# Performance work log

Hardware: AMD Instinct MI355X
Metric: run time of the kernel (lower is better)

## Reference

```python
import jax, jax.numpy as jnp
import numpy as np

N = 100000   # nodes
E = 1600000  # edges
G = 64       # graphs in batch
H, C = 8, 16 # heads, per-head channels
HID = H * C  # 128
EMB, BBOX, TOK, REL = 256, 32, 151, 51
IN0 = EMB + BBOX  # 288
NEG_SLOPE = 0.2
BN_EPS = 1e-5


def setup_inputs() -> dict:
    key = jax.random.key(0)
    ks = jax.random.split(key, 32)
    f = lambda i, shape: jax.random.normal(ks[i], shape, dtype=jnp.float32) * 0.05
    inp = {}
    inp["tok_id"] = jax.random.randint(ks[0], (N,), 0, TOK)
    inp["bbox"] = jax.random.normal(ks[1], (N, 4), dtype=jnp.float32)
    inp["edge_index"] = jax.random.randint(ks[2], (2, E), 0, N)
    inp["edge_attr"] = jax.random.randint(ks[3], (E,), 0, REL)
    inp["batch"] = jnp.sort(jax.random.randint(ks[4], (N,), 0, G))
    inp["tok_emb"] = f(5, (TOK, EMB))
    inp["bbox_W"] = f(6, (4, BBOX)); inp["bbox_b"] = f(7, (BBOX,))
    inp["rel_emb"] = f(8, (REL, C))
    # layer 0 (in_dim 288 -> 128)
    inp["Wl0"] = f(9, (IN0, HID));  inp["bl0"] = f(10, (HID,))
    inp["Wr0"] = f(11, (IN0, HID)); inp["br0"] = f(12, (HID,))
    inp["We0"] = f(13, (C, HID));   inp["att0"] = f(14, (H, C))
    inp["bias0"] = f(15, (HID,))
    inp["gamma0"] = jnp.ones((HID,), jnp.float32); inp["beta0"] = jnp.zeros((HID,), jnp.float32)
    # layers 1..2 stacked (128 -> 128)
    inp["WlS"] = f(16, (2, HID, HID)); inp["blS"] = f(17, (2, HID))
    inp["WrS"] = f(18, (2, HID, HID)); inp["brS"] = f(19, (2, HID))
    inp["WeS"] = f(20, (2, C, HID));   inp["attS"] = f(21, (2, H, C))
    inp["biasS"] = f(22, (2, HID))
    inp["gammaS"] = jnp.ones((2, HID), jnp.float32); inp["betaS"] = jnp.zeros((2, HID), jnp.float32)
    return inp


def gatv2_layer(x, src, dst, e_emb, Wl, bl, Wr, br, We, att, bias):
    """GATv2Conv: gather -> leaky_relu attention -> segment softmax -> scatter."""
    xl = (x @ Wl + bl).reshape(-1, H, C)   # source transform [N,H,C]
    xr = (x @ Wr + br).reshape(-1, H, C)   # target transform [N,H,C]
    ee = (e_emb @ We).reshape(-1, H, C)    # edge transform  [E,H,C]
    m = jax.nn.leaky_relu(xl[src] + xr[dst] + ee, NEG_SLOPE)  # [E,H,C]
    logits = jnp.einsum('ehc,hc->eh', m, att)                 # [E,H]
    amax = jax.ops.segment_max(logits, dst, num_segments=N)   # [N,H]
    p = jnp.exp(logits - amax[dst])
    denom = jax.ops.segment_sum(p, dst, num_segments=N)       # [N,H]
    alpha = p / jnp.maximum(denom[dst], 1e-16)                # [E,H]
    out = jax.ops.segment_sum(alpha[..., None] * xl[src], dst, num_segments=N)  # [N,H,C]
    return out.reshape(-1, HID) + bias


def batch_norm(x, gamma, beta):
    mu = jnp.mean(x, axis=0)
    var = jnp.var(x, axis=0)
    return gamma * (x - mu) * jax.lax.rsqrt(var + BN_EPS) + beta


def reference(tok_id, bbox, edge_index, edge_attr, batch,
              tok_emb, bbox_W, bbox_b, rel_emb,
              Wl0, bl0, Wr0, br0, We0, att0, bias0, gamma0, beta0,
              WlS, blS, WrS, brS, WeS, attS, biasS, gammaS, betaS):
    src, dst = edge_index[0], edge_index[1]
    x = jnp.concatenate([tok_emb[tok_id], bbox @ bbox_W + bbox_b], axis=-1)  # [N,288]
    e_emb = rel_emb[edge_attr]  # [E,16]
    h = batch_norm(jax.nn.relu(
        gatv2_layer(x, src, dst, e_emb, Wl0, bl0, Wr0, br0, We0, att0, bias0)),
        gamma0, beta0)
    for i in range(2):
        h = h + batch_norm(jax.nn.relu(
            gatv2_layer(h, src, dst, e_emb, WlS[i], blS[i], WrS[i], brS[i], WeS[i], attS[i], biasS[i])),
            gammaS[i], betaS[i])
    # global mean pool over graphs
    sums = jax.ops.segment_sum(h, batch, num_segments=G)
    counts = jax.ops.segment_sum(jnp.ones((h.shape[0],), h.dtype), batch, num_segments=G)
    return sums / jnp.maximum(counts, 1.0)[:, None]  # [G,128]
```

## Files before the change

kernel.cpp:

```cpp
#include <hip/hip_runtime.h>

#define N_NODES 100000
#define N_PAD   100096
#define N_EDGES 1600000
#define NGRAPH  64
#define NHEAD   8
#define NCH     16
#define HID     128
#define IN0     288
#define NREL    51
#define EMB     256
#define NBBOX   32
#define NTOK    151
#define NEG_SLOPE 0.2f
#define EPS_BN  1e-5f
#define AGG_BLOCKS 2048
#define POOL_BLOCKS 1024
#define SENT 0x03F00000u
#define SENT_MIN ((uint)(NREL) << 20)
#define L2E 1.4426950408889634f

typedef unsigned int uint;
typedef unsigned short ushort;

typedef __bf16 bf16_t;
typedef bf16_t bfx8 __attribute__((ext_vector_type(8)));
typedef float  fx4  __attribute__((ext_vector_type(4)));
typedef float  v2f  __attribute__((ext_vector_type(2)));

__device__ __forceinline__ ushort f2bf(float f) {
  uint u = __float_as_uint(f);
  u += 0x7fffu + ((u >> 16) & 1u);
  return (ushort)(u >> 16);
}
__device__ __forceinline__ float bf2f(uint u) { return __uint_as_float(u << 16); }
__device__ __forceinline__ v2f up2(uint u) {
  v2f r;
  r.x = __uint_as_float(u << 16);
  r.y = __uint_as_float(u & 0xffff0000u);
  return r;
}
__device__ __forceinline__ void unpack8(uint4 u, float* f) {
  f[0] = __uint_as_float(u.x << 16); f[1] = __uint_as_float(u.x & 0xffff0000u);
  f[2] = __uint_as_float(u.y << 16); f[3] = __uint_as_float(u.y & 0xffff0000u);
  f[4] = __uint_as_float(u.z << 16); f[5] = __uint_as_float(u.z & 0xffff0000u);
  f[6] = __uint_as_float(u.w << 16); f[7] = __uint_as_float(u.w & 0xffff0000u);
}

__device__ __forceinline__ float w0cat(const float* Wl0, const float* Wr0, int c, int j) {
  return (j < 128) ? Wl0[c * 128 + j] : Wr0[c * 128 + (j - 128)];
}

#define S0 (2 * 256 * HID)
#define S1 (3 * NREL * HID)
#define S2 (3 * 256)
#define S3 (NTOK * 256)
#define S4 (4 * 256)
#define S5 (256)
#define PREP_TOT (S0 + S1 + S2 + S3 + S4 + S5)
__global__ void se_prep(const float* __restrict__ Wl0, const float* __restrict__ Wr0,
                        const float* __restrict__ WlS, const float* __restrict__ WrS,
                        const float* __restrict__ rel_emb, const float* __restrict__ We0,
                        const float* __restrict__ WeS,
                        const float* __restrict__ bl0, const float* __restrict__ br0,
                        const float* __restrict__ blS, const float* __restrict__ brS,
                        const float* __restrict__ tok_emb, const float* __restrict__ bbox_W,
                        const float* __restrict__ bbox_b,
                        ushort* __restrict__ WST, float* __restrict__ eetab,
                        float* __restrict__ biascat,
                        float* __restrict__ T, float* __restrict__ F, float* __restrict__ cvec) {
  int i = blockIdx.x * 256 + threadIdx.x;
  if (i < S0) {
    int li = i >> 15;
    int rem = i & 32767;
    int j = rem >> 7, k = rem & 127;
    float v = (j < 128) ? WlS[(li * 128 + k) * 128 + j] : WrS[(li * 128 + k) * 128 + (j - 128)];
    WST[(li * 256 + j) * 128 + k] = f2bf(v);
    return;
  }
  i -= S0;
  if (i < S1) {
    int li = i / (NREL * HID);
    int rem = i - li * (NREL * HID);
    int r = rem >> 7, j = rem & 127;
    const float* We = (li == 0) ? We0 : (WeS + (li - 1) * NCH * HID);
    float s = 0.f;
#pragma unroll
    for (int c = 0; c < NCH; c++) s += rel_emb[r * NCH + c] * We[c * HID + j];
    eetab[li * (NREL * HID) + rem] = s;
    return;
  }
  i -= S1;
  if (i < S2) {
    int li = i >> 8, j = i & 255;
    const float* bl = (li == 0) ? bl0 : (blS + (li - 1) * HID);
    const float* br = (li == 0) ? br0 : (brS + (li - 1) * HID);
    biascat[i] = (j < 128) ? bl[j] : br[j - 128];
    return;
  }
  i -= S2;
  if (i < S3) {
    int t = i >> 8, j = i & 255;
    float s = 0.f;
    for (int c = 0; c < EMB; c++) s += tok_emb[t * EMB + c] * w0cat(Wl0, Wr0, c, j);
    T[i] = s;
    return;
  }
  i -= S3;
  if (i < S4) {
    int r = i >> 8, j = i & 255;
    float s = 0.f;
#pragma unroll
    for (int b = 0; b < NBBOX; b++) s += bbox_W[r * NBBOX + b] * w0cat(Wl0, Wr0, EMB + b, j);
    F[i] = s;
    return;
  }
  i -= S4;
  if (i < S5) {
    int j = i;
    float s = (j < 128) ? bl0[j] : br0[j - 128];
#pragma unroll
    for (int b = 0; b < NBBOX; b++) s += bbox_b[b] * w0cat(Wl0, Wr0, EMB + b, j);
    cvec[j] = s;
  }
}

__global__ void se_xform0(const int* __restrict__ tok_id, const float* __restrict__ bbox,
                          const float* __restrict__ T, const float* __restrict__ F,
                          const float* __restrict__ cvec, ushort* __restrict__ xlxr) {
  int idx = blockIdx.x * 256 + threadIdx.x;
  if (idx >= N_NODES * 32) return;
  const int n = idx >> 5, k = idx & 31;
  const int j0 = k * 8;
  const int t = tok_id[n];
  const float4 bb = *(const float4*)(bbox + (size_t)n * 4);
  float o[8];
#pragma unroll
  for (int h = 0; h < 2; h++) {
    const float4 tv = *(const float4*)(T + t * 256 + j0 + 4 * h);
    const float4 cv = *(const float4*)(cvec + j0 + 4 * h);
    const float4 f0 = *(const float4*)(F + 0 * 256 + j0 + 4 * h);
    const float4 f1 = *(const float4*)(F + 1 * 256 + j0 + 4 * h);
    const float4 f2 = *(const float4*)(F + 2 * 256 + j0 + 4 * h);
    const float4 f3 = *(const float4*)(F + 3 * 256 + j0 + 4 * h);
    o[4 * h + 0] = tv.x + cv.x + bb.x * f0.x + bb.y * f1.x + bb.z * f2.x + bb.w * f3.x;
    o[4 * h + 1] = tv.y + cv.y + bb.x * f0.y + bb.y * f1.y + bb.z * f2.y + bb.w * f3.y;
    o[4 * h + 2] = tv.z + cv.z + bb.x * f0.z + bb.y * f1.z + bb.z * f2.z + bb.w * f3.z;
    o[4 * h + 3] = tv.w + cv.w + bb.x * f0.w + bb.y * f1.w + bb.z * f2.w + bb.w * f3.w;
  }
  uint4 p;
  p.x = ((uint)f2bf(o[1]) << 16) | f2bf(o[0]);
  p.y = ((uint)f2bf(o[3]) << 16) | f2bf(o[2]);
  p.z = ((uint)f2bf(o[5]) << 16) | f2bf(o[4]);
  p.w = ((uint)f2bf(o[7]) << 16) | f2bf(o[6]);
  ((uint4*)xlxr)[idx] = p;
}

__global__ void se_hist(const int* __restrict__ ei, int* __restrict__ deg) {
  int e = blockIdx.x * 256 + threadIdx.x;
  if (e < N_EDGES) atomicAdd(&deg[ei[N_EDGES + e]], 1);
}
__global__ __launch_bounds__(1024) void se_scanA(const int* __restrict__ deg,
                                                 int* __restrict__ offs, int* __restrict__ bsum) {
  __shared__ int s[1024];
  const int tid = threadIdx.x;
  const int i = blockIdx.x * 1024 + tid;
  int v = (i < N_NODES) ? ((deg[i] + 3) & ~3) : 0;
  s[tid] = v;
  __syncthreads();
  for (int d = 1; d < 1024; d <<= 1) {
    int t = (tid >= d) ? s[tid - d] : 0;
    __syncthreads();
    s[tid] += t;
    __syncthreads();
  }
  if (i < N_NODES) offs[i] = s[tid] - v;
  if (tid == 1023) bsum[blockIdx.x] = s[1023];
}
__global__ __launch_bounds__(128) void se_scanB(int* __restrict__ bsum, int nb) {
  __shared__ int s[128];
  const int t = threadIdx.x;
  int v = (t < nb) ? bsum[t] : 0;
  s[t] = v;
  __syncthreads();
  for (int d = 1; d < 128; d <<= 1) {
    int u = (t >= d) ? s[t - d] : 0;
    __syncthreads();
    s[t] += u;
    __syncthreads();
  }
  if (t < nb) bsum[t] = s[t] - v;
}
__global__ __launch_bounds__(1024) void se_scanC(int* __restrict__ offs, const int* __restrict__ bsum) {
  int i = blockIdx.x * 1024 + threadIdx.x;
  if (i < N_NODES) offs[i] += bsum[blockIdx.x];
}
__global__ void se_padfill(const int* __restrict__ deg, const int* __restrict__ offs,
                           uint* __restrict__ csrp, int2* __restrict__ rowinfo) {
  int n = blockIdx.x * 256 + threadIdx.x;
  if (n >= N_NODES) return;
  const int d = deg[n];
  const int o = offs[n];
  rowinfo[n] = make_int2(o, (d + 3) >> 2);
  const int s = o + d;
  const int c = ((d + 3) & ~3) - d;
  for (int j = 0; j < c; j++) csrp[s + j] = SENT;
  if (n == N_NODES - 1) {
    const int e = o + ((d + 3) & ~3);
    for (int j = 0; j < 64; j++) csrp[e + j] = SENT;
  }
}
__global__ void se_scatter(const int* __restrict__ ei, const int* __restrict__ eattr,
                           const int* __restrict__ offs, int* __restrict__ cur,
                           uint* __restrict__ csrp) {
  int e = blockIdx.x * 256 + threadIdx.x;
  if (e < N_EDGES) {
    int d = ei[N_EDGES + e];
    int p = offs[d] + atomicAdd(&cur[d], 1);
    csrp[p] = (uint)ei[e] | ((uint)eattr[e] << 20);
  }
}

template <int K>
__global__ __launch_bounds__(256) void se_gemm(const ushort* __restrict__ A,
                                               const ushort* __restrict__ BT,
                                               const float* __restrict__ bias,
                                               ushort* __restrict__ C) {
  __shared__ __align__(16) ushort As[128 * 32];
  __shared__ __align__(16) ushort Bs[128 * 32];
  const int tid = threadIdx.x;
  const int w = tid >> 6, l = tid & 63;
  const int wr = w >> 1, wc = w & 1;
  const int m0 = blockIdx.x * 128, n0 = blockIdx.y * 128;
  fx4 acc[4][4];
#pragma unroll
  for (int i = 0; i < 4; i++)
#pragma unroll
    for (int j = 0; j < 4; j++) acc[i][j] = fx4{0.f, 0.f, 0.f, 0.f};

  for (int k0 = 0; k0 < K; k0 += 32) {
#pragma unroll
    for (int ch = 0; ch < 2; ch++) {
      const int t = tid + ch * 256;
      const int r = t >> 2, c = (t & 3) << 3;
      const ushort* ga = A + (size_t)(m0 + r) * K + (k0 + c);
      ushort* la = As + (size_t)(ch * 256 + w * 64) * 8;
      __builtin_amdgcn_global_load_lds((const __attribute__((address_space(1))) void*)ga,
                                       (__attribute__((address_space(3))) void*)la, 16, 0, 0);
      const ushort* gb = BT + (size_t)(n0 + r) * K + (k0 + c);
      ushort* lb = Bs + (size_t)(ch * 256 + w * 64) * 8;
      __builtin_amdgcn_global_load_lds((const __attribute__((address_space(1))) void*)gb,
                                       (__attribute__((address_space(3))) void*)lb, 16, 0, 0);
    }
    __syncthreads();
    bfx8 af[4], bfr[4];
#pragma unroll
    for (int i = 0; i < 4; i++) {
      af[i]  = *(const bfx8*)(As + ((wr * 64 + i * 16 + (l & 15)) * 32 + ((l >> 4) * 8)));
      bfr[i] = *(const bfx8*)(Bs + ((wc * 64 + i * 16 + (l & 15)) * 32 + ((l >> 4) * 8)));
    }
#pragma unroll
    for (int i = 0; i < 4; i++)
#pragma unroll
      for (int j = 0; j < 4; j++)
        acc[i][j] = __builtin_amdgcn_mfma_f32_16x16x32_bf16(af[i], bfr[j], acc[i][j], 0, 0, 0);
    __syncthreads();
  }
#pragma unroll
  for (int i = 0; i < 4; i++) {
    const int rbase = m0 + wr * 64 + i * 16 + ((l >> 4) << 2);
#pragma unroll
    for (int j = 0; j < 4; j++) {
      const int col = n0 + wc * 64 + j * 16 + (l & 15);
      const float bz = bias[col];
#pragma unroll
      for (int r2 = 0; r2 < 4; r2++) {
        const int row = rbase + r2;
        if (row < N_NODES) C[(size_t)row * 256 + col] = f2bf(acc[i][j][r2] + bz);
      }
    }
  }
}

__global__ __launch_bounds__(256) void se_agg(const uint4* __restrict__ xlxr4,
                                              const uint* __restrict__ csrp,
                                              const int2* __restrict__ rowinfo,
                                              const float* __restrict__ eetab,
                                              const float* __restrict__ att,
                                              const float* __restrict__ bias,
                                              ushort* __restrict__ y, float* __restrict__ partial) {
  __shared__ ushort ee[64 * HID];
  __shared__ float bstat[256];
  const int tid = threadIdx.x, w = tid >> 6, l = tid & 63;
  const int g = l >> 4, k = l & 15;
  for (int i = tid; i < 64 * HID; i += 256) {
    const int r = i >> 7;
    ee[i] = (r < NREL) ? f2bf(eetab[i]) : (ushort)0;
  }
  bstat[tid] = 0.f;
  __syncthreads();
  v2f a1v[4], a2v[4];
  {
    const float* ap = att + (k >> 1) * NCH + (k & 1) * 8;
#pragma unroll
    for (int q = 0; q < 4; q++) {
      a1v[q] = v2f{ap[2 * q] * (0.6f * L2E), ap[2 * q + 1] * (0.6f * L2E)};
      a2v[q] = v2f{ap[2 * q] * (0.4f * L2E), ap[2 * q + 1] * (0.4f * L2E)};
    }
  }
  v2f sv[4], qv[4];
#pragma unroll
  for (int q = 0; q < 4; q++) { sv[q] = v2f{0.f, 0.f}; qv[q] = v2f{0.f, 0.f}; }
  const v2f zero = v2f{0.f, 0.f};

  const int stride = gridDim.x * 4;
  for (int n = blockIdx.x * 4 + w; n < N_NODES; n += stride) {
    const int2 ri = rowinfo[n];
    const uint* rowp = csrp + ri.x + g;
    const int nit = ri.y;
    v2f xrv[4];
    {
      const uint4 xru = xlxr4[(uint)n * 32u + 16u + (uint)k];
      xrv[0] = up2(xru.x); xrv[1] = up2(xru.y); xrv[2] = up2(xru.z); xrv[3] = up2(xru.w);
    }
    float den = 0.f;
    v2f acc[4];
#pragma unroll
    for (int q = 0; q < 4; q++) acc[q] = zero;

    uint eA = SENT, eB = SENT;
    uint4 xlv = uint4{0u, 0u, 0u, 0u};
    if (nit > 0) {
      eA = rowp[0];
      xlv = xlxr4[(eA & 0xFFFFFu) * 32u + (uint)k];
      if (nit > 1) eB = rowp[4];
    }
    for (int i = 0; i < nit; ++i) {
      const uint ec = eA;
      const uint4 xc = xlv;
      eA = eB;
      if (i + 1 < nit) xlv = xlxr4[(eA & 0xFFFFFu) * 32u + (uint)k];
      if (i + 2 < nit) eB = rowp[4 * (i + 2)];
      const uint4 eeu = *(const uint4*)(ee + (ec >> 20) * HID + k * 8);
      v2f sd1 = zero, sd2 = zero;
      v2f xls[4];
      {
        const uint xcu[4] = {xc.x, xc.y, xc.z, xc.w};
        const uint eu[4] = {eeu.x, eeu.y, eeu.z, eeu.w};
#pragma unroll
        for (int q = 0; q < 4; q++) {
          const v2f xl = up2(xcu[q]);
          const v2f m = xl + xrv[q] + up2(eu[q]);
          sd1 += m * a1v[q];
          sd2 += __builtin_elementwise_abs(m) * a2v[q];
          xls[q] = xl;
        }
      }
      float s = sd1.x + sd1.y + sd2.x + sd2.y;
      s += __shfl_xor(s, 1);
      s = (ec >= SENT_MIN) ? -1e30f : s;
      const float p = exp2f(s);
      den += p;
      const v2f pp = v2f{p, p};
#pragma unroll
      for (int q = 0; q < 4; q++) acc[q] += pp * xls[q];
    }
    den += __shfl_xor(den, 16);
    den += __shfl_xor(den, 32);
#pragma unroll
    for (int q = 0; q < 4; q++) {
      acc[q].x += __shfl_xor(acc[q].x, 16); acc[q].x += __shfl_xor(acc[q].x, 32);
      acc[q].y += __shfl_xor(acc[q].y, 16); acc[q].y += __shfl_xor(acc[q].y, 32);
    }
    if (g == 0) {
      const float r = 1.f / fmaxf(den, 1e-16f);
      const v2f rr = v2f{r, r};
      const float4 b0 = ((const float4*)bias)[k * 2];
      const float4 b1 = ((const float4*)bias)[k * 2 + 1];
      const v2f bv[4] = {v2f{b0.x, b0.y}, v2f{b0.z, b0.w}, v2f{b1.x, b1.y}, v2f{b1.z, b1.w}};
      v2f ov[4];
#pragma unroll
      for (int q = 0; q < 4; q++) {
        ov[q] = __builtin_elementwise_max(acc[q] * rr + bv[q], zero);
        sv[q] += ov[q];
        qv[q] += ov[q] * ov[q];
      }
      uint4 p4;
      p4.x = ((uint)f2bf(ov[0].y) << 16) | f2bf(ov[0].x);
      p4.y = ((uint)f2bf(ov[1].y) << 16) | f2bf(ov[1].x);
      p4.z = ((uint)f2bf(ov[2].y) << 16) | f2bf(ov[2].x);
      p4.w = ((uint)f2bf(ov[3].y) << 16) | f2bf(ov[3].x);
      ((uint4*)y)[(size_t)n * 16 + k] = p4;
    }
  }
  if (l < 16) {
#pragma unroll
    for (int q = 0; q < 4; q++) {
      unsafeAtomicAdd(&bstat[k * 8 + 2 * q], sv[q].x);
      unsafeAtomicAdd(&bstat[k * 8 + 2 * q + 1], sv[q].y);
      unsafeAtomicAdd(&bstat[128 + k * 8 + 2 * q], qv[q].x);
      unsafeAtomicAdd(&bstat[128 + k * 8 + 2 * q + 1], qv[q].y);
    }
  }
  __syncthreads();
  partial[(size_t)tid * AGG_BLOCKS + blockIdx.x] = bstat[tid];
}

__global__ __launch_bounds__(256) void se_stats(const float* __restrict__ partial, float* __restrict__ musig) {
  __shared__ float red[256];
  const int ch = blockIdx.x, tid = threadIdx.x;
  float s = 0.f;
  for (int i = tid; i < AGG_BLOCKS; i += 256) s += partial[ch * AGG_BLOCKS + i];
  red[tid] = s; __syncthreads();
  for (int o = 128; o > 0; o >>= 1) { if (tid < o) red[tid] += red[tid + o]; __syncthreads(); }
  const float sum = red[0]; __syncthreads();
  float q = 0.f;
  for (int i = tid; i < AGG_BLOCKS; i += 256) q += partial[(128 + ch) * AGG_BLOCKS + i];
  red[tid] = q; __syncthreads();
  for (int o = 128; o > 0; o >>= 1) { if (tid < o) red[tid] += red[tid + o]; __syncthreads(); }
  if (tid == 0) {
    const float mean = sum / (float)N_NODES;
    const float var = red[0] / (float)N_NODES - mean * mean;
    musig[ch] = mean;
    musig[128 + ch] = rsqrtf(var + EPS_BN);
  }
}

__global__ void se_bn(const ushort* __restrict__ y, const float* __restrict__ musig,
                      const float* __restrict__ gamma, const float* __restrict__ beta,
                      ushort* __restrict__ h_bf, int residual) {
  int idx = blockIdx.x * 256 + threadIdx.x;
  if (idx >= N_NODES * 16) return;
  const int k = idx & 15;
  const uint4 yv = ((const uint4*)y)[idx];
  float f[8];
  unpack8(yv, f);
  const float4 mu0 = ((const float4*)musig)[k * 2],         mu1 = ((const float4*)musig)[k * 2 + 1];
  const float4 rs0 = ((const float4*)(musig + 128))[k * 2], rs1 = ((const float4*)(musig + 128))[k * 2 + 1];
  const float4 g0  = ((const float4*)gamma)[k * 2],         g1  = ((const float4*)gamma)[k * 2 + 1];
  const float4 b0  = ((const float4*)beta)[k * 2],          b1  = ((const float4*)beta)[k * 2 + 1];
  float v[8];
  v[0] = g0.x * (f[0] - mu0.x) * rs0.x + b0.x;
  v[1] = g0.y * (f[1] - mu0.y) * rs0.y + b0.y;
  v[2] = g0.z * (f[2] - mu0.z) * rs0.z + b0.z;
  v[3] = g0.w * (f[3] - mu0.w) * rs0.w + b0.w;
  v[4] = g1.x * (f[4] - mu1.x) * rs1.x + b1.x;
  v[5] = g1.y * (f[5] - mu1.y) * rs1.y + b1.y;
  v[6] = g1.z * (f[6] - mu1.z) * rs1.z + b1.z;
  v[7] = g1.w * (f[7] - mu1.w) * rs1.w + b1.w;
  if (residual) {
    const uint4 ho = ((const uint4*)h_bf)[idx];
    float fr[8];
    unpack8(ho, fr);
#pragma unroll
    for (int j = 0; j < 8; j++) v[j] += fr[j];
  }
  uint4 p4;
  p4.x = ((uint)f2bf(v[1]) << 16) | f2bf(v[0]);
  p4.y = ((uint)f2bf(v[3]) << 16) | f2bf(v[2]);
  p4.z = ((uint)f2bf(v[5]) << 16) | f2bf(v[4]);
  p4.w = ((uint)f2bf(v[7]) << 16) | f2bf(v[6]);
  ((uint4*)h_bf)[idx] = p4;
}

__global__ __launch_bounds__(256) void se_pool(const ushort* __restrict__ h_bf,
                                               const int* __restrict__ batch,
                                               float* __restrict__ pool) {
  const int tid = threadIdx.x, w = tid >> 6, l = tid & 63;
  const int wid = blockIdx.x * 4 + w;
  const int nw = gridDim.x * 4;
  const int chunk = (N_NODES + nw - 1) / nw;
  const int start = wid * chunk;
  const int end = min(N_NODES, start + chunk);
  float a0 = 0.f, a1 = 0.f;
  int cg = -1, cnt = 0;
  for (int n = start; n < end; ++n) {
    const int gg = batch[n];
    if (gg != cg) {
      if (cg >= 0) {
        unsafeAtomicAdd(&pool[cg * HID + 2 * l], a0);
        unsafeAtomicAdd(&pool[cg * HID + 2 * l + 1], a1);
        if (l == 0) unsafeAtomicAdd(&pool[NGRAPH * HID + cg], (float)cnt);
      }
      a0 = 0.f; a1 = 0.f; cnt = 0; cg = gg;
    }
    const uint u = ((const uint*)h_bf)[(size_t)n * 64 + l];
    a0 += bf2f(u & 0xffffu);
    a1 += __uint_as_float(u & 0xffff0000u);
    cnt++;
  }
  if (cg >= 0) {
    unsafeAtomicAdd(&pool[cg * HID + 2 * l], a0);
    unsafeAtomicAdd(&pool[cg * HID + 2 * l + 1], a1);
    if (l == 0) unsafeAtomicAdd(&pool[NGRAPH * HID + cg], (float)cnt);
  }
}
__global__ void se_poolfin(const float* __restrict__ pool, float* __restrict__ out) {
  int idx = blockIdx.x * 256 + threadIdx.x;
  if (idx < NGRAPH * HID) {
    int g = idx >> 7;
    out[idx] = pool[idx] / fmaxf(pool[NGRAPH * HID + g], 1.f);
  }
}

extern "C" void kernel_launch(void* const* d_in, const int* in_sizes, int n_in,
                              void* d_out, int out_size, void* d_ws, size_t ws_size,
                              hipStream_t stream) {
  (void)in_sizes; (void)n_in; (void)out_size; (void)ws_size;
  const int*   tok_id  = (const int*)d_in[0];
  const float* bbox    = (const float*)d_in[1];
  const int*   ei      = (const int*)d_in[2];
  const int*   eattr   = (const int*)d_in[3];
  const int*   batch   = (const int*)d_in[4];
  const float* tok_emb = (const float*)d_in[5];
  const float* bbox_W  = (const float*)d_in[6];
  const float* bbox_b  = (const float*)d_in[7];
  const float* rel_emb = (const float*)d_in[8];
  const float* Wl0  = (const float*)d_in[9];
  const float* bl0  = (const float*)d_in[10];
  const float* Wr0  = (const float*)d_in[11];
  const float* br0  = (const float*)d_in[12];
  const float* We0  = (const float*)d_in[13];
  const float* att0 = (const float*)d_in[14];
  const float* bias0  = (const float*)d_in[15];
  const float* gamma0 = (const float*)d_in[16];
  const float* beta0  = (const float*)d_in[17];
  const float* WlS  = (const float*)d_in[18];
  const float* blS  = (const float*)d_in[19];
  const float* WrS  = (const float*)d_in[20];
  const float* brS  = (const float*)d_in[21];
  const float* WeS  = (const float*)d_in[22];
  const float* attS = (const float*)d_in[23];
  const float* biasS  = (const float*)d_in[24];
  const float* gammaS = (const float*)d_in[25];
  const float* betaS  = (const float*)d_in[26];
  float* out = (float*)d_out;

  char* ws = (char*)d_ws;
  size_t off = 0;
  auto alloc = [&](size_t bytes) -> char* {
    char* p = ws + off;
    off = (off + bytes + 255) & ~(size_t)255;
    return p;
  };
  ushort* xlxr = (ushort*)alloc((size_t)N_PAD * 256 * 2);
  ushort* y    = (ushort*)alloc((size_t)N_NODES * HID * 2);
  ushort* h_bf = (ushort*)alloc((size_t)N_PAD * HID * 2);
  ushort* WST  = (ushort*)alloc((size_t)2 * 256 * HID * 2);
  float*  eetab   = (float*)alloc((size_t)3 * NREL * HID * 4);
  float*  biascat = (float*)alloc((size_t)3 * 256 * 4);
  float*  T    = (float*)alloc((size_t)NTOK * 256 * 4);
  float*  F    = (float*)alloc((size_t)4 * 256 * 4);
  float*  cvec = (float*)alloc((size_t)256 * 4);
  int* deg  = (int*)alloc((size_t)N_NODES * 4);
  int* offs = (int*)alloc((size_t)(N_NODES + 1) * 4);
  int* cur  = (int*)alloc((size_t)N_NODES * 4);
  int* bsum = (int*)alloc(128 * 4);
  int2* rowinfo = (int2*)alloc((size_t)N_NODES * 8);
  uint* csrp = (uint*)alloc((size_t)(N_EDGES + 3 * N_NODES + 256) * 4);
  float* partial = (float*)alloc((size_t)256 * AGG_BLOCKS * 4);
  float* musig   = (float*)alloc(256 * 4);
  float* pool    = (float*)alloc((size_t)(NGRAPH * HID + NGRAPH) * 4);

  hipMemsetAsync(deg, 0, (size_t)N_NODES * 4, stream);
  hipMemsetAsync(cur, 0, (size_t)N_NODES * 4, stream);
  hipMemsetAsync(pool, 0, (size_t)(NGRAPH * HID + NGRAPH) * 4, stream);

  se_prep<<<(PREP_TOT + 255) / 256, 256, 0, stream>>>(
      Wl0, Wr0, WlS, WrS, rel_emb, We0, WeS, bl0, br0, blS, brS,
      tok_emb, bbox_W, bbox_b, WST, eetab, biascat, T, F, cvec);
  se_hist<<<(N_EDGES + 255) / 256, 256, 0, stream>>>(ei, deg);
  se_scanA<<<98, 1024, 0, stream>>>(deg, offs, bsum);
  se_scanB<<<1, 128, 0, stream>>>(bsum, 98);
  se_scanC<<<98, 1024, 0, stream>>>(offs, bsum);
  se_padfill<<<(N_NODES + 255) / 256, 256, 0, stream>>>(deg, offs, csrp, rowinfo);
  se_scatter<<<(N_EDGES + 255) / 256, 256, 0, stream>>>(ei, eattr, offs, cur, csrp);

  se_xform0<<<(N_NODES * 32 + 255) / 256, 256, 0, stream>>>(tok_id, bbox, T, F, cvec, xlxr);
  se_agg<<<AGG_BLOCKS, 256, 0, stream>>>((const uint4*)xlxr, csrp, rowinfo,
                                         eetab, att0, bias0, y, partial);
  se_stats<<<128, 256, 0, stream>>>(partial, musig);
  se_bn<<<(N_NODES * 16 + 255) / 256, 256, 0, stream>>>(y, musig, gamma0, beta0, h_bf, 0);

  for (int li = 0; li < 2; ++li) {
    se_gemm<HID><<<dim3(N_PAD / 128, 2), 256, 0, stream>>>(h_bf, WST + (size_t)li * 256 * HID,
                                                           biascat + (li + 1) * 256, xlxr);
    se_agg<<<AGG_BLOCKS, 256, 0, stream>>>((const uint4*)xlxr, csrp, rowinfo,
                                           eetab + (size_t)(li + 1) * NREL * HID,
                                           attS + (size_t)li * NHEAD * NCH,
                                           biasS + (size_t)li * HID, y, partial);
    se_stats<<<128, 256, 0, stream>>>(partial, musig);
    se_bn<<<(N_NODES * 16 + 255) / 256, 256, 0, stream>>>(y, musig, gammaS + (size_t)li * HID,
                                                          betaS + (size_t)li * HID, h_bf, 1);
  }

  se_pool<<<POOL_BLOCKS, 256, 0, stream>>>(h_bf, batch, pool);
  se_poolfin<<<32, 256, 0, stream>>>(pool, out);
}
```

Before: 828.2 us.

## Use fp32 edge table and output, direct leaky-relu, merged memsets

The aggregation kernel now keeps the edge-embedding table in shared memory as fp32 instead of bf16. It computes leaky_relu directly as max(m, 0.2m) instead of the abs-based split into two accumulators, and unrolls the edge loop by two. The intermediate y buffer is stored as fp32, so the batch-norm kernel reads floats instead of unpacking bf16. The three workspace memsets are merged into one by placing the zeroed buffers next to each other. This trims ALU work in the inner loop and removes two memset launches, at the cost of twice the y traffic and more shared memory per block, which may lower occupancy.

```diff
diff --git a/kernel.cpp b/kernel.cpp
--- a/kernel.cpp
+++ b/kernel.cpp
@@ -288,25 +288,22 @@
                                               const float* __restrict__ eetab,
                                               const float* __restrict__ att,
                                               const float* __restrict__ bias,
-                                              ushort* __restrict__ y, float* __restrict__ partial) {
-  __shared__ ushort ee[64 * HID];
+                                              float* __restrict__ y, float* __restrict__ partial) {
+  __shared__ float ee[64 * HID];
   __shared__ float bstat[256];
   const int tid = threadIdx.x, w = tid >> 6, l = tid & 63;
   const int g = l >> 4, k = l & 15;
   for (int i = tid; i < 64 * HID; i += 256) {
     const int r = i >> 7;
-    ee[i] = (r < NREL) ? f2bf(eetab[i]) : (ushort)0;
+    ee[i] = (r < NREL) ? eetab[i] : 0.f;
   }
   bstat[tid] = 0.f;
   __syncthreads();
-  v2f a1v[4], a2v[4];
+  v2f av[4];
   {
     const float* ap = att + (k >> 1) * NCH + (k & 1) * 8;
 #pragma unroll
-    for (int q = 0; q < 4; q++) {
-      a1v[q] = v2f{ap[2 * q] * (0.6f * L2E), ap[2 * q + 1] * (0.6f * L2E)};
-      a2v[q] = v2f{ap[2 * q] * (0.4f * L2E), ap[2 * q + 1] * (0.4f * L2E)};
-    }
+    for (int q = 0; q < 4; q++) av[q] = v2f{ap[2 * q] * L2E, ap[2 * q + 1] * L2E};
   }
   v2f sv[4], qv[4];
 #pragma unroll
@@ -335,28 +332,32 @@
       xlv = xlxr4[(eA & 0xFFFFFu) * 32u + (uint)k];
       if (nit > 1) eB = rowp[4];
     }
+#pragma unroll 2
     for (int i = 0; i < nit; ++i) {
       const uint ec = eA;
       const uint4 xc = xlv;
       eA = eB;
       if (i + 1 < nit) xlv = xlxr4[(eA & 0xFFFFFu) * 32u + (uint)k];
       if (i + 2 < nit) eB = rowp[4 * (i + 2)];
-      const uint4 eeu = *(const uint4*)(ee + (ec >> 20) * HID + k * 8);
-      v2f sd1 = zero, sd2 = zero;
+      const float* eerow = ee + (ec >> 20) * HID + k * 8;
+      const float4 e0v = *(const float4*)(eerow);
+      const float4 e1v = *(const float4*)(eerow + 4);
+      const v2f eef[4] = {v2f{e0v.x, e0v.y}, v2f{e0v.z, e0v.w},
+                          v2f{e1v.x, e1v.y}, v2f{e1v.z, e1v.w}};
+      v2f sd = zero;
       v2f xls[4];
       {
         const uint xcu[4] = {xc.x, xc.y, xc.z, xc.w};
-        const uint eu[4] = {eeu.x, eeu.y, eeu.z, eeu.w};
 #pragma unroll
         for (int q = 0; q < 4; q++) {
           const v2f xl = up2(xcu[q]);
-          const v2f m = xl + xrv[q] + up2(eu[q]);
-          sd1 += m * a1v[q];
-          sd2 += __builtin_elementwise_abs(m) * a2v[q];
+          const v2f m = xl + xrv[q] + eef[q];
+          const v2f lk = __builtin_elementwise_max(m, NEG_SLOPE * m);
+          sd += lk * av[q];
           xls[q] = xl;
         }
       }
-      float s = sd1.x + sd1.y + sd2.x + sd2.y;
+      float s = sd.x + sd.y;
       s += __shfl_xor(s, 1);
       s = (ec >= SENT_MIN) ? -1e30f : s;
       const float p = exp2f(s);
@@ -385,12 +386,9 @@
         sv[q] += ov[q];
         qv[q] += ov[q] * ov[q];
       }
-      uint4 p4;
-      p4.x = ((uint)f2bf(ov[0].y) << 16) | f2bf(ov[0].x);
-      p4.y = ((uint)f2bf(ov[1].y) << 16) | f2bf(ov[1].x);
-      p4.z = ((uint)f2bf(ov[2].y) << 16) | f2bf(ov[2].x);
-      p4.w = ((uint)f2bf(ov[3].y) << 16) | f2bf(ov[3].x);
-      ((uint4*)y)[(size_t)n * 16 + k] = p4;
+      float4* yp = (float4*)y + (size_t)n * 32 + (size_t)k * 2;
+      yp[0] = make_float4(ov[0].x, ov[0].y, ov[1].x, ov[1].y);
+      yp[1] = make_float4(ov[2].x, ov[2].y, ov[3].x, ov[3].y);
     }
   }
   if (l < 16) {
@@ -426,28 +424,27 @@
   }
 }
 
-__global__ void se_bn(const ushort* __restrict__ y, const float* __restrict__ musig,
+__global__ void se_bn(const float* __restrict__ y, const float* __restrict__ musig,
                       const float* __restrict__ gamma, const float* __restrict__ beta,
                       ushort* __restrict__ h_bf, int residual) {
   int idx = blockIdx.x * 256 + threadIdx.x;
   if (idx >= N_NODES * 16) return;
   const int k = idx & 15;
-  const uint4 yv = ((const uint4*)y)[idx];
-  float f[8];
-  unpack8(yv, f);
+  const float4 y0 = ((const float4*)y)[(size_t)idx * 2];
+  const float4 y1 = ((const float4*)y)[(size_t)idx * 2 + 1];
   const float4 mu0 = ((const float4*)musig)[k * 2],         mu1 = ((const float4*)musig)[k * 2 + 1];
   const float4 rs0 = ((const float4*)(musig + 128))[k * 2], rs1 = ((const float4*)(musig + 128))[k * 2 + 1];
   const float4 g0  = ((const float4*)gamma)[k * 2],         g1  = ((const float4*)gamma)[k * 2 + 1];
   const float4 b0  = ((const float4*)beta)[k * 2],          b1  = ((const float4*)beta)[k * 2 + 1];
   float v[8];
-  v[0] = g0.x * (f[0] - mu0.x) * rs0.x + b0.x;
-  v[1] = g0.y * (f[1] - mu0.y) * rs0.y + b0.y;
-  v[2] = g0.z * (f[2] - mu0.z) * rs0.z + b0.z;
-  v[3] = g0.w * (f[3] - mu0.w) * rs0.w + b0.w;
-  v[4] = g1.x * (f[4] - mu1.x) * rs1.x + b1.x;
-  v[5] = g1.y * (f[5] - mu1.y) * rs1.y + b1.y;
-  v[6] = g1.z * (f[6] - mu1.z) * rs1.z + b1.z;
-  v[7] = g1.w * (f[7] - mu1.w) * rs1.w + b1.w;
+  v[0] = g0.x * (y0.x - mu0.x) * rs0.x + b0.x;
+  v[1] = g0.y * (y0.y - mu0.y) * rs0.y + b0.y;
+  v[2] = g0.z * (y0.z - mu0.z) * rs0.z + b0.z;
+  v[3] = g0.w * (y0.w - mu0.w) * rs0.w + b0.w;
+  v[4] = g1.x * (y1.x - mu1.x) * rs1.x + b1.x;
+  v[5] = g1.y * (y1.y - mu1.y) * rs1.y + b1.y;
+  v[6] = g1.z * (y1.z - mu1.z) * rs1.z + b1.z;
+  v[7] = g1.w * (y1.w - mu1.w) * rs1.w + b1.w;
   if (residual) {
     const uint4 ho = ((const uint4*)h_bf)[idx];
     float fr[8];
@@ -544,7 +541,7 @@
     return p;
   };
   ushort* xlxr = (ushort*)alloc((size_t)N_PAD * 256 * 2);
-  ushort* y    = (ushort*)alloc((size_t)N_NODES * HID * 2);
+  float*  y    = (float*)alloc((size_t)N_NODES * HID * 4);
   ushort* h_bf = (ushort*)alloc((size_t)N_PAD * HID * 2);
   ushort* WST  = (ushort*)alloc((size_t)2 * 256 * HID * 2);
   float*  eetab   = (float*)alloc((size_t)3 * NREL * HID * 4);
@@ -552,19 +549,19 @@
   float*  T    = (float*)alloc((size_t)NTOK * 256 * 4);
   float*  F    = (float*)alloc((size_t)4 * 256 * 4);
   float*  cvec = (float*)alloc((size_t)256 * 4);
-  int* deg  = (int*)alloc((size_t)N_NODES * 4);
+  char*  z0   = ws + off;
+  int*   deg  = (int*)alloc((size_t)N_NODES * 4);
+  int*   cur  = (int*)alloc((size_t)N_NODES * 4);
+  float* pool = (float*)alloc((size_t)(NGRAPH * HID + NGRAPH) * 4);
+  size_t zlen = (size_t)((ws + off) - z0);
   int* offs = (int*)alloc((size_t)(N_NODES + 1) * 4);
-  int* cur  = (int*)alloc((size_t)N_NODES * 4);
   int* bsum = (int*)alloc(128 * 4);
   int2* rowinfo = (int2*)alloc((size_t)N_NODES * 8);
   uint* csrp = (uint*)alloc((size_t)(N_EDGES + 3 * N_NODES + 256) * 4);
   float* partial = (float*)alloc((size_t)256 * AGG_BLOCKS * 4);
   float* musig   = (float*)alloc(256 * 4);
-  float* pool    = (float*)alloc((size_t)(NGRAPH * HID + NGRAPH) * 4);
-
-  hipMemsetAsync(deg, 0, (size_t)N_NODES * 4, stream);
-  hipMemsetAsync(cur, 0, (size_t)N_NODES * 4, stream);
-  hipMemsetAsync(pool, 0, (size_t)(NGRAPH * HID + NGRAPH) * 4, stream);
+
+  hipMemsetAsync(z0, 0, zlen, stream);
 
   se_prep<<<(PREP_TOT + 255) / 256, 256, 0, stream>>>(
       Wl0, Wr0, WlS, WrS, rel_emb, We0, WeS, bl0, br0, blS, brS,
```

Measured after the change: 814.7 us. No clear change (-1.6%).
